# Kernel optimization log

Measured on AMD Instinct MI355X. Metric: run time of the kernel, lower is better.

## Reference

```python
import jax, jax.numpy as jnp
import numpy as np

R, E, N = 16, 4096, 262144  # relations, entities, labeled triplets


def setup_inputs() -> dict:
    key = jax.random.key(0)
    k1, k2, k3, k4, k5 = jax.random.split(key, 5)
    return {
        "predicted_values": jax.random.normal(k1, (R, E, E), dtype=jnp.float32),
        "rel_idx": jax.random.randint(k2, (N,), 0, R, dtype=jnp.int32),
        "e1_idx": jax.random.randint(k3, (N,), 0, E, dtype=jnp.int32),
        "e2_idx": jax.random.randint(k4, (N,), 0, E, dtype=jnp.int32),
        "labels": jax.random.randint(k5, (N,), 0, 2, dtype=jnp.int32),
    }


def reference(predicted_values, rel_idx, e1_idx, e2_idx, labels):
    # Batched version of the per-sample loop: gather score for each triplet,
    # apply sigmoid, accumulate label-weighted terms, normalize by
    # (1 + #negatives) * N with an overall -1 factor.
    scores = predicted_values[rel_idx, e1_idx, e2_idx]  # [N]
    sig = jax.nn.sigmoid(scores)
    lab = labels.astype(sig.dtype)
    neg = jnp.sum(labels == 0).astype(sig.dtype)
    total = jnp.sum(lab * sig + (1.0 - lab) * (1.0 - sig))
    n = jnp.asarray(labels.shape[0], sig.dtype)
    loss = -total / ((1.0 + neg) * n)
    return loss.reshape(1)
```

## Files before the change

kernel.cpp:

```cpp
#include <hip/hip_runtime.h>


#define NBLK 256

__global__ __launch_bounds__(256) void loss_partial_kernel(
        const float* __restrict__ pv,
        const int* __restrict__ rel_idx,
        const int* __restrict__ e1_idx,
        const int* __restrict__ e2_idx,
        const int* __restrict__ labels,
        float* __restrict__ ws_sum,
        int*   __restrict__ ws_neg) {
    int t = blockIdx.x * blockDim.x + threadIdx.x;

    int4 r4 = reinterpret_cast<const int4*>(rel_idx)[t];
    int4 a4 = reinterpret_cast<const int4*>(e1_idx)[t];
    int4 b4 = reinterpret_cast<const int4*>(e2_idx)[t];
    int4 L4 = reinterpret_cast<const int4*>(labels)[t];

    const int* rp = &r4.x; const int* ap = &a4.x;
    const int* bp = &b4.x; const int* Lp = &L4.x;
    float x[4];
    #pragma unroll
    for (int k = 0; k < 4; ++k) {
        size_t idx = ((((size_t)rp[k] << 12) | (size_t)ap[k]) << 12) | (size_t)bp[k];
        x[k] = pv[idx];
    }

    float term = 0.0f;
    int negc = 0;
    #pragma unroll
    for (int k = 0; k < 4; ++k) {
        float sx = Lp[k] ? -x[k] : x[k];
        term += 1.0f / (1.0f + expf(sx));
        negc += (Lp[k] == 0) ? 1 : 0;
    }

    #pragma unroll
    for (int off = 32; off > 0; off >>= 1) {
        term += __shfl_down(term, off, 64);
        negc += __shfl_down(negc, off, 64);
    }

    __shared__ float sterm[4];
    __shared__ int   sneg[4];
    int lane = threadIdx.x & 63;
    int wid  = threadIdx.x >> 6;
    if (lane == 0) { sterm[wid] = term; sneg[wid] = negc; }
    __syncthreads();

    if (threadIdx.x == 0) {
        ws_sum[blockIdx.x] = sterm[0] + sterm[1] + sterm[2] + sterm[3];
        ws_neg[blockIdx.x] = sneg[0] + sneg[1] + sneg[2] + sneg[3];
    }
}

__global__ __launch_bounds__(256) void loss_final_kernel(
        const float* __restrict__ ws_sum,
        const int*   __restrict__ ws_neg,
        float* __restrict__ out, int n) {
    float term = ws_sum[threadIdx.x];
    int   negc = ws_neg[threadIdx.x];
    #pragma unroll
    for (int off = 32; off > 0; off >>= 1) {
        term += __shfl_down(term, off, 64);
        negc += __shfl_down(negc, off, 64);
    }
    __shared__ float sterm[4];
    __shared__ int   sneg[4];
    int lane = threadIdx.x & 63;
    int wid  = threadIdx.x >> 6;
    if (lane == 0) { sterm[wid] = term; sneg[wid] = negc; }
    __syncthreads();
    if (threadIdx.x == 0) {
        double total = (double)(sterm[0] + sterm[1] + sterm[2] + sterm[3]);
        double neg   = (double)(sneg[0] + sneg[1] + sneg[2] + sneg[3]);
        out[0] = (float)(-total / ((1.0 + neg) * (double)n));
    }
}

extern "C" void kernel_launch(void* const* d_in, const int* in_sizes, int n_in,
                              void* d_out, int out_size, void* d_ws, size_t ws_size,
                              hipStream_t stream) {
    const float* pv      = (const float*)d_in[0];
    const int*   rel_idx = (const int*)d_in[1];
    const int*   e1_idx  = (const int*)d_in[2];
    const int*   e2_idx  = (const int*)d_in[3];
    const int*   labels  = (const int*)d_in[4];
    float* out = (float*)d_out;

    float* ws_sum = (float*)d_ws;
    int*   ws_neg = (int*)((char*)d_ws + NBLK * sizeof(float));

    int n = in_sizes[1];

    loss_partial_kernel<<<NBLK, 256, 0, stream>>>(pv, rel_idx, e1_idx, e2_idx,
                                                  labels, ws_sum, ws_neg);
    loss_final_kernel<<<1, 256, 0, stream>>>(ws_sum, ws_neg, out, n);
}
```

Before: 11.63 us.

## Fuse final reduction into partial kernel via last-block atomic counter

Replaces the separate final-reduction kernel launch with a last-block-done pattern: each block publishes its partials with release stores and increments a two-level atomic counter (8 groups, then a global counter), and the last block performs the final reduction. This removes one kernel launch and the gap between the two kernels. In exchange it adds a hipMemsetAsync to zero the counters each call, which is still a separate stream operation, plus atomic traffic per block.

After: 23.98 us. 2.06x slower.

```diff
diff --git a/kernel.cpp b/kernel.cpp
--- a/kernel.cpp
+++ b/kernel.cpp
@@ -2,16 +2,22 @@
 
 
 #define NBLK 256
+#define TPB  256
+#define NGRP 8
+#define GRP_SZ (NBLK / NGRP)
 
-__global__ __launch_bounds__(256) void loss_partial_kernel(
+__global__ __launch_bounds__(256) void loss_fused_kernel(
         const float* __restrict__ pv,
         const int* __restrict__ rel_idx,
         const int* __restrict__ e1_idx,
         const int* __restrict__ e2_idx,
         const int* __restrict__ labels,
+        float* __restrict__ out,
+        unsigned* __restrict__ cnt,
         float* __restrict__ ws_sum,
-        int*   __restrict__ ws_neg) {
-    int t = blockIdx.x * blockDim.x + threadIdx.x;
+        int*   __restrict__ ws_neg,
+        int n) {
+    int t = blockIdx.x * TPB + threadIdx.x;
 
     int4 r4 = reinterpret_cast<const int4*>(rel_idx)[t];
     int4 a4 = reinterpret_cast<const int4*>(e1_idx)[t];
@@ -44,38 +50,52 @@
 
     __shared__ float sterm[4];
     __shared__ int   sneg[4];
+    __shared__ int   s_last;
     int lane = threadIdx.x & 63;
     int wid  = threadIdx.x >> 6;
     if (lane == 0) { sterm[wid] = term; sneg[wid] = negc; }
     __syncthreads();
 
     if (threadIdx.x == 0) {
-        ws_sum[blockIdx.x] = sterm[0] + sterm[1] + sterm[2] + sterm[3];
-        ws_neg[blockIdx.x] = sneg[0] + sneg[1] + sneg[2] + sneg[3];
+        float bt = sterm[0] + sterm[1] + sterm[2] + sterm[3];
+        int   bc = sneg[0] + sneg[1] + sneg[2] + sneg[3];
+        __hip_atomic_store(&ws_sum[blockIdx.x], bt,
+                           __ATOMIC_RELEASE, __HIP_MEMORY_SCOPE_AGENT);
+        __hip_atomic_store(&ws_neg[blockIdx.x], bc,
+                           __ATOMIC_RELEASE, __HIP_MEMORY_SCOPE_AGENT);
+        s_last = 0;
+        int g = blockIdx.x & (NGRP - 1);
+        unsigned o1 = __hip_atomic_fetch_add(&cnt[g * 32], 1u,
+                           __ATOMIC_ACQ_REL, __HIP_MEMORY_SCOPE_AGENT);
+        if (o1 == GRP_SZ - 1) {
+            unsigned o2 = __hip_atomic_fetch_add(&cnt[256], 1u,
+                               __ATOMIC_ACQ_REL, __HIP_MEMORY_SCOPE_AGENT);
+            if (o2 == NGRP - 1) s_last = 1;
+        }
     }
-}
+    __syncthreads();
 
-__global__ __launch_bounds__(256) void loss_final_kernel(
-        const float* __restrict__ ws_sum,
-        const int*   __restrict__ ws_neg,
-        float* __restrict__ out, int n) {
-    float term = ws_sum[threadIdx.x];
-    int   negc = ws_neg[threadIdx.x];
-    #pragma unroll
-    for (int off = 32; off > 0; off >>= 1) {
-        term += __shfl_down(term, off, 64);
-        negc += __shfl_down(negc, off, 64);
-    }
-    __shared__ float sterm[4];
-    __shared__ int   sneg[4];
-    int lane = threadIdx.x & 63;
-    int wid  = threadIdx.x >> 6;
-    if (lane == 0) { sterm[wid] = term; sneg[wid] = negc; }
-    __syncthreads();
-    if (threadIdx.x == 0) {
-        double total = (double)(sterm[0] + sterm[1] + sterm[2] + sterm[3]);
-        double neg   = (double)(sneg[0] + sneg[1] + sneg[2] + sneg[3]);
-        out[0] = (float)(-total / ((1.0 + neg) * (double)n));
+    if (s_last) {
+        (void)__hip_atomic_load(&cnt[256], __ATOMIC_ACQUIRE,
+                                __HIP_MEMORY_SCOPE_AGENT);
+        int i = threadIdx.x;
+        float ft = __hip_atomic_load(&ws_sum[i], __ATOMIC_RELAXED,
+                                     __HIP_MEMORY_SCOPE_AGENT);
+        int   fc = __hip_atomic_load(&ws_neg[i], __ATOMIC_RELAXED,
+                                     __HIP_MEMORY_SCOPE_AGENT);
+        #pragma unroll
+        for (int off = 32; off > 0; off >>= 1) {
+            ft += __shfl_down(ft, off, 64);
+            fc += __shfl_down(fc, off, 64);
+        }
+        __syncthreads();
+        if (lane == 0) { sterm[wid] = ft; sneg[wid] = fc; }
+        __syncthreads();
+        if (threadIdx.x == 0) {
+            double total = (double)(sterm[0] + sterm[1] + sterm[2] + sterm[3]);
+            double neg   = (double)(sneg[0] + sneg[1] + sneg[2] + sneg[3]);
+            out[0] = (float)(-total / ((1.0 + neg) * (double)n));
+        }
     }
 }
 
@@ -89,12 +109,14 @@
     const int*   labels  = (const int*)d_in[4];
     float* out = (float*)d_out;
 
-    float* ws_sum = (float*)d_ws;
-    int*   ws_neg = (int*)((char*)d_ws + NBLK * sizeof(float));
+    unsigned* cnt    = (unsigned*)d_ws;
+    float*    ws_sum = (float*)((char*)d_ws + 2048);
+    int*      ws_neg = (int*)((char*)d_ws + 3072);
 
     int n = in_sizes[1];
 
-    loss_partial_kernel<<<NBLK, 256, 0, stream>>>(pv, rel_idx, e1_idx, e2_idx,
-                                                  labels, ws_sum, ws_neg);
-    loss_final_kernel<<<1, 256, 0, stream>>>(ws_sum, ws_neg, out, n);
+    hipMemsetAsync(d_ws, 0, 2048, stream);
+    loss_fused_kernel<<<NBLK, TPB, 0, stream>>>(pv, rel_idx, e1_idx, e2_idx,
+                                                labels, out, cnt, ws_sum,
+                                                ws_neg, n);
 }
```
